# Kernel optimization log

Hardware: AMD Instinct MI355X
Metric: run time of the kernel (lower is better)

The kernel has to match this reference:

```python
import jax, jax.numpy as jnp
import numpy as np

H = 4  # attention heads


def gat_layer(x, src, dst, W, a_src, a_dst, b, N):
    """PyG-style GATConv (concat=True, negative_slope=0.2, eval-mode dropout)."""
    h = (x @ W).reshape(N, H, -1)                       # [N,H,C]
    es = jnp.einsum('nhc,hc->nh', h, a_src)             # per-node src score
    ed = jnp.einsum('nhc,hc->nh', h, a_dst)             # per-node dst score
    e = jax.nn.leaky_relu(es[src] + ed[dst], negative_slope=0.2)  # [E,H]
    # segment softmax over incoming edges of each destination node
    emax = jax.ops.segment_max(e, dst, num_segments=N)
    ee = jnp.exp(e - emax[dst])
    denom = jax.ops.segment_sum(ee, dst, num_segments=N)
    alpha = ee / (denom[dst] + 1e-16)                   # [E,H]
    out = jax.ops.segment_sum(h[src] * alpha[..., None], dst, num_segments=N)
    return out.reshape(N, -1) + b                        # [N,H*C]


def setup_inputs() -> dict:
    key = jax.random.key(0)
    ks = jax.random.split(key, 13)
    N, E, D, Q = 50000, 800000, 256, 8
    HID, OUT = 256, 256
    Ch, Co = HID // H, OUT // H
    inp = {}
    inp['x'] = jax.random.normal(ks[0], (N, D), dtype=jnp.float32)
    inp['edge_index'] = jax.random.randint(ks[1], (2, E), 0, N, dtype=jnp.int64)
    inp['query_embedding'] = jax.random.normal(ks[2], (Q, OUT), dtype=jnp.float32)
    # layer 1: input_dim -> heads * (hidden_dim//heads)
    inp['W1'] = jax.random.normal(ks[3], (D, HID), dtype=jnp.float32) / np.sqrt(D).astype(np.float32)
    inp['a_src1'] = jax.random.normal(ks[4], (H, Ch), dtype=jnp.float32) / np.sqrt(Ch).astype(np.float32)
    inp['a_dst1'] = jax.random.normal(ks[5], (H, Ch), dtype=jnp.float32) / np.sqrt(Ch).astype(np.float32)
    inp['b1'] = jnp.zeros((HID,), dtype=jnp.float32)
    # layer 2: hidden_dim -> heads * (output_dim//heads)
    inp['W2'] = jax.random.normal(ks[6], (HID, OUT), dtype=jnp.float32) / np.sqrt(HID).astype(np.float32)
    inp['a_src2'] = jax.random.normal(ks[7], (H, Co), dtype=jnp.float32) / np.sqrt(Co).astype(np.float32)
    inp['a_dst2'] = jax.random.normal(ks[8], (H, Co), dtype=jnp.float32) / np.sqrt(Co).astype(np.float32)
    inp['b2'] = jnp.zeros((OUT,), dtype=jnp.float32)
    # node classifier over concat([query, node]) -> 1 (intended Linear(2*OUT, 1))
    inp['Wc'] = jax.random.normal(ks[9], (2 * OUT, 1), dtype=jnp.float32) / np.sqrt(2 * OUT).astype(np.float32)
    inp['bc'] = jnp.zeros((1,), dtype=jnp.float32)
    return inp


def reference(x, edge_index, query_embedding, W1, a_src1, a_dst1, b1,
              W2, a_src2, a_dst2, b2, Wc, bc):
    N = x.shape[0]
    loops = jnp.arange(N, dtype=edge_index.dtype)        # GATConv add_self_loops=True
    src = jnp.concatenate([edge_index[0], loops])
    dst = jnp.concatenate([edge_index[1], loops])
    h = jax.nn.relu(gat_layer(x, src, dst, W1, a_src1, a_dst1, b1, N))
    emb = gat_layer(h, src, dst, W2, a_src2, a_dst2, b2, N)  # [N, OUT]
    D = emb.shape[1]
    # scores[q,n] = Linear(concat(query[q], emb[n])) — computed without
    # materializing the [Q,N,2D] concat (identical math).
    q_part = query_embedding @ Wc[:D] + bc               # [Q,1]
    n_part = emb @ Wc[D:]                                # [N,1]
    node_scores = q_part[:, 0][:, None] + n_part[:, 0][None, :]  # [Q,N]
    return emb, node_scores
```

## Files before the change

### kernel.cpp

```cpp
#include <hip/hip_runtime.h>

typedef unsigned short u16;
typedef unsigned int   u32;
typedef __attribute__((ext_vector_type(8))) short short8v;
typedef __attribute__((ext_vector_type(8))) unsigned short us8;
typedef __attribute__((ext_vector_type(4))) float f32x4;

static __device__ __forceinline__ float bf2f(u16 u){ union{u32 i; float f;} v; v.i=(u32)u<<16; return v.f; }
static __device__ __forceinline__ u16 f2bf(float f){ union{float f; u32 i;} u; u.f=f; u32 r=u.i+0x7FFFu+((u.i>>16)&1u); return (u16)(r>>16); }
static __device__ __forceinline__ u32 cvtpk(float lo, float hi){
  u32 r; asm("v_cvt_pk_bf16_f32 %0, %1, %2" : "=v"(r) : "v"(lo), "v"(hi)); return r;
}

static __device__ __forceinline__ float ld1(const void* p, size_t i, int f32){
  return f32 ? ((const float*)p)[i] : bf2f(((const u16*)p)[i]);
}
static __device__ __forceinline__ float4 ld4(const void* p, size_t i, int f32){
  if (f32) return *((const float4*)((const float*)p + i));
  ushort4 v = *((const ushort4*)((const u16*)p + i));
  return make_float4(bf2f(v.x), bf2f(v.y), bf2f(v.z), bf2f(v.w));
}
static __device__ __forceinline__ void st4(void* p, size_t i, float4 v, int f32){
  if (f32) *((float4*)((float*)p + i)) = v;
  else { ushort4 o; o.x=f2bf(v.x); o.y=f2bf(v.y); o.z=f2bf(v.z); o.w=f2bf(v.w); *((ushort4*)((u16*)p + i)) = o; }
}
static __device__ __forceinline__ void st1(void* p, size_t i, float v, int f32){
  if (f32) ((float*)p)[i] = v; else ((u16*)p)[i] = f2bf(v);
}
static __device__ __forceinline__ int lde(const int* ei, size_t i, int i64){
  return i64 ? ei[2*i] : ei[i];
}
static __device__ __forceinline__ int clampi(int v, int lo, int hi){ return v<lo?lo:(v>hi?hi:v); }

__global__ void detect_kernel(const u32* __restrict__ x, const int* __restrict__ ei,
                              int* __restrict__ flags){
  __shared__ int cnt[2];
  int t = threadIdx.x;
  if (t < 2) cnt[t] = 0;
  __syncthreads();
  int good = 0;
  for (int i = t; i < 4096; i += 256){
    u32 e = (x[i] >> 7) & 0xFFu;
    if (e >= 90u && e <= 150u) good++;
  }
  atomicAdd(&cnt[0], good);
  int nzodd = 0;
  for (int i = t; i < 2048; i += 256){
    if (ei[2*i+1] != 0) nzodd++;
  }
  atomicAdd(&cnt[1], nzodd);
  __syncthreads();
  if (t == 0){
    flags[0] = (cnt[0] < 2867) ? 1 : 0;
    flags[1] = (cnt[1] == 0) ? 1 : 0;
  }
}

__global__ __launch_bounds__(256) void convx_kernel(const void* __restrict__ x,
    u16* __restrict__ out, long total, const int* __restrict__ flags){
  if (!flags[0]) return;
  long i = ((long)blockIdx.x*256 + threadIdx.x) * 8;
  if (i >= total) return;
  const float* xf = (const float*)x + i;
  float4 v0 = *(const float4*)xf, v1 = *(const float4*)(xf+4);
  union{ u32 w[4]; us8 v; } pk;
  pk.w[0] = cvtpk(v0.x, v0.y); pk.w[1] = cvtpk(v0.z, v0.w);
  pk.w[2] = cvtpk(v1.x, v1.y); pk.w[3] = cvtpk(v1.z, v1.w);
  *(us8*)(out + i) = pk.v;
}

__global__ void count_kernel(const int* __restrict__ ei, int E, int N,
                             int* __restrict__ deg, const int* __restrict__ flags){
  int i64 = flags[1];
  int i = blockIdx.x*blockDim.x + threadIdx.x;
  int Et = E + N;
  if (i < Et){
    int d = (i < E) ? clampi(lde(ei, (size_t)E + i, i64), 0, N-1) : (i - E);
    atomicAdd(&deg[d], 1);
  }
}

__global__ __launch_bounds__(256) void scan1_kernel(const int* __restrict__ deg,
    int* __restrict__ offs, int* __restrict__ bsum, int N){
  __shared__ int sm[256];
  int t = threadIdx.x;
  int i = blockIdx.x*256 + t;
  int v = (i < N) ? deg[i] : 0;
  sm[t] = v; __syncthreads();
  #pragma unroll
  for (int off = 1; off < 256; off <<= 1){
    int u = (t >= off) ? sm[t-off] : 0;
    __syncthreads();
    sm[t] += u;
    __syncthreads();
  }
  if (i < N) offs[i] = sm[t] - v;
  if (t == 255) bsum[blockIdx.x] = sm[255];
}

__global__ __launch_bounds__(1024) void scan2_kernel(const int* __restrict__ bsum,
    int* __restrict__ bpre, int NB){
  __shared__ int sm[1024];
  int t = threadIdx.x;
  int v = (t < NB) ? bsum[t] : 0;
  sm[t] = v; __syncthreads();
  #pragma unroll
  for (int off = 1; off < 1024; off <<= 1){
    int u = (t >= off) ? sm[t-off] : 0;
    __syncthreads();
    sm[t] += u;
    __syncthreads();
  }
  if (t < NB) bpre[t] = sm[t] - v;
  if (t == 1023) bpre[NB] = sm[1023];
}

__global__ __launch_bounds__(256) void scan3_kernel(int* __restrict__ offs,
    int* __restrict__ cursor, const int* __restrict__ bpre, int N, int NB){
  int i = blockIdx.x*256 + threadIdx.x;
  if (i < N){
    int v = offs[i] + bpre[blockIdx.x];
    offs[i] = v; cursor[i] = v;
  }
  if (i == 0) offs[N] = bpre[NB];
}

__global__ void scatter_kernel(const int* __restrict__ ei, int E, int N,
    int* __restrict__ cursor, int* __restrict__ csr_boff, const int* __restrict__ flags){
  int i64 = flags[1];
  int i = blockIdx.x*blockDim.x + threadIdx.x;
  int Et = E + N;
  if (i < Et){
    int s, d;
    if (i < E){
      s = clampi(lde(ei, i, i64), 0, N-1);
      d = clampi(lde(ei, (size_t)E + i, i64), 0, N-1);
    } else { s = i - E; d = s; }
    int p = atomicAdd(&cursor[d], 1);
    csr_boff[p] = s * 512;
  }
}

__global__ __launch_bounds__(256) void prep_kernel(const void* __restrict__ B1,
    const void* __restrict__ B2, u16* __restrict__ BT1, u16* __restrict__ BT2,
    const void* __restrict__ query, const void* __restrict__ Wc, const void* __restrict__ bc,
    float* __restrict__ qp, int Q, const int* __restrict__ flags){
  int f32 = flags[0];
  int bid = blockIdx.x;
  if (bid < 32){
    const void* B = (bid >= 16) ? B2 : B1;
    u16* BT = (bid >= 16) ? BT2 : BT1;
    int rem = bid & 15;
    int k0 = (rem >> 2)*64, c0 = (rem & 3)*64;
    __shared__ u16 tile[64][65];
    int r0 = threadIdx.x >> 6, c = threadIdx.x & 63;
    for (int r = r0; r < 64; r += 4)
      tile[r][c] = f32 ? f2bf(((const float*)B)[(size_t)(k0+r)*256 + c0 + c])
                       : ((const u16*)B)[(size_t)(k0+r)*256 + c0 + c];
    __syncthreads();
    for (int j = r0; j < 64; j += 4)
      BT[(size_t)(c0+j)*256 + k0 + c] = tile[c][j];
  } else {
    int q = threadIdx.x >> 5, ln = threadIdx.x & 31;
    if (q >= Q) return;
    float s = 0.f;
    for (int j = ln; j < 256; j += 32) s += ld1(query, q*256 + j, f32) * ld1(Wc, j, f32);
    #pragma unroll
    for (int off = 16; off; off >>= 1) s += __shfl_down(s, off, 32);
    if (ln == 0) qp[q] = s + ld1(bc, 0, f32);
  }
}

__global__ __launch_bounds__(256, 4) void gemm_mfma(const u16* __restrict__ A0,
    const u16* __restrict__ A1, const u16* __restrict__ BT, u16* __restrict__ C,
    int M, int aIsInput, const int* __restrict__ flags, float* __restrict__ es,
    float* __restrict__ ed, const void* __restrict__ a_src, const void* __restrict__ a_dst){
  const u16* A16 = (aIsInput && flags[0]) ? A1 : A0;
  int f32 = flags[0];
  int tid = threadIdx.x;
  int wn = tid >> 6, lane = tid & 63;
  int l15 = lane & 15, l4 = lane >> 4;
  int row0 = blockIdx.x * 64;
  int arow[4];
  #pragma unroll
  for (int mi = 0; mi < 4; mi++)
    arow[mi] = min(row0 + mi*16 + l15, M-1);
  const u16* Bb = BT + (size_t)(wn*64 + l15)*256 + 8*l4;
  f32x4 acc[4][4] = {};
  #pragma unroll
  for (int k0 = 0; k0 < 256; k0 += 32){
    short8v a[4], b[4];
    #pragma unroll
    for (int mi = 0; mi < 4; mi++)
      a[mi] = *(const short8v*)(A16 + (size_t)arow[mi]*256 + k0 + 8*l4);
    #pragma unroll
    for (int ni = 0; ni < 4; ni++)
      b[ni] = *(const short8v*)(Bb + (size_t)ni*16*256 + k0);
    #pragma unroll
    for (int mi = 0; mi < 4; mi++)
      #pragma unroll
      for (int ni = 0; ni < 4; ni++)
        acc[mi][ni] = __builtin_amdgcn_mfma_f32_16x16x32_bf16(a[mi], b[ni], acc[mi][ni], 0, 0, 0);
  }
  #pragma unroll
  for (int mi = 0; mi < 4; mi++){
    #pragma unroll
    for (int ni = 0; ni < 4; ni++){
      #pragma unroll
      for (int r = 0; r < 4; r++){
        int row = row0 + mi*16 + l4*4 + r;
        int col = wn*64 + ni*16 + l15;
        if (row < M) C[(size_t)row*256 + col] = f2bf(acc[mi][ni][r]);
      }
    }
  }
  float as_[4], ad_[4];
  #pragma unroll
  for (int ni = 0; ni < 4; ni++){
    as_[ni] = ld1(a_src, wn*64 + ni*16 + l15, f32);
    ad_[ni] = ld1(a_dst, wn*64 + ni*16 + l15, f32);
  }
  #pragma unroll
  for (int mi = 0; mi < 4; mi++){
    #pragma unroll
    for (int r = 0; r < 4; r++){
      float pe = acc[mi][0][r]*as_[0] + acc[mi][1][r]*as_[1]
               + acc[mi][2][r]*as_[2] + acc[mi][3][r]*as_[3];
      float pd = acc[mi][0][r]*ad_[0] + acc[mi][1][r]*ad_[1]
               + acc[mi][2][r]*ad_[2] + acc[mi][3][r]*ad_[3];
      #pragma unroll
      for (int off = 1; off < 16; off <<= 1){
        pe += __shfl_xor(pe, off, 64);
        pd += __shfl_xor(pd, off, 64);
      }
      if (l15 == 0){
        int row = row0 + mi*16 + l4*4 + r;
        if (row < M){
          es[(size_t)row*4 + wn] = pe;
          ed[(size_t)row*4 + wn] = pd;
        }
      }
    }
  }
}

__global__ __launch_bounds__(256) void agg_kernel(const u16* __restrict__ h,
    const int* __restrict__ csr_boff, const int* __restrict__ offs,
    const float* __restrict__ es, const float* __restrict__ ed, int N,
    const void* __restrict__ bias, void* __restrict__ out, int do_relu, int outIsOutput,
    const int* __restrict__ flags, const void* __restrict__ Wc,
    const float* __restrict__ qp, int Q){
  int f32in = flags[0];
  int of32  = outIsOutput ? flags[0] : 0;
  int ln = threadIdx.x & 63;
  int n = blockIdx.x*4 + (threadIdx.x >> 6);
  if (n >= N) return;
  int beg = offs[n], end = offs[n+1];
  int hd = ln >> 4, c0 = ln*4;
  int hd4 = hd*4;
  size_t coff = (size_t)c0*2;
  const char* hbase = (const char*)h;
  const char* ebase = (const char*)es;
  float edn = ed[(size_t)n*4 + hd];
  float a0=0.f, a1=0.f, a2=0.f, a3=0.f, ws=0.f;
  int i = beg;
  for (; i + 8 <= end; i += 8){
    int bo[8]; float x[8]; ushort4 hv[8];
    #pragma unroll
    for (int j = 0; j < 8; j++) bo[j] = csr_boff[i+j];
    #pragma unroll
    for (int j = 0; j < 8; j++) x[j] = *(const float*)(ebase + (bo[j] >> 5) + hd4);
    #pragma unroll
    for (int j = 0; j < 8; j++) hv[j] = *(const ushort4*)(hbase + bo[j] + coff);
    #pragma unroll
    for (int j = 0; j < 8; j++){
      float t = x[j] + edn; t = (t > 0.f) ? t : 0.2f*t; t = fminf(t, 60.f);
      float w = __expf(t);
      a0 += w*bf2f(hv[j].x); a1 += w*bf2f(hv[j].y);
      a2 += w*bf2f(hv[j].z); a3 += w*bf2f(hv[j].w);
      ws += w;
    }
  }
  for (; i + 4 <= end; i += 4){
    int bo[4]; float x[4]; ushort4 hv[4];
    #pragma unroll
    for (int j = 0; j < 4; j++) bo[j] = csr_boff[i+j];
    #pragma unroll
    for (int j = 0; j < 4; j++) x[j] = *(const float*)(ebase + (bo[j] >> 5) + hd4);
    #pragma unroll
    for (int j = 0; j < 4; j++) hv[j] = *(const ushort4*)(hbase + bo[j] + coff);
    #pragma unroll
    for (int j = 0; j < 4; j++){
      float t = x[j] + edn; t = (t > 0.f) ? t : 0.2f*t; t = fminf(t, 60.f);
      float w = __expf(t);
      a0 += w*bf2f(hv[j].x); a1 += w*bf2f(hv[j].y);
      a2 += w*bf2f(hv[j].z); a3 += w*bf2f(hv[j].w);
      ws += w;
    }
  }
  for (; i < end; i++){
    int bo = csr_boff[i];
    float t = *(const float*)(ebase + (bo >> 5) + hd4) + edn;
    t = (t > 0.f) ? t : 0.2f*t; t = fminf(t, 60.f);
    float w = __expf(t);
    ushort4 hv = *(const ushort4*)(hbase + bo + coff);
    a0 += w*bf2f(hv.x); a1 += w*bf2f(hv.y);
    a2 += w*bf2f(hv.z); a3 += w*bf2f(hv.w);
    ws += w;
  }
  float inv = 1.f / (ws + 1e-16f);
  float4 bv = ld4(bias, c0, f32in);
  float4 ov = make_float4(a0*inv + bv.x, a1*inv + bv.y, a2*inv + bv.z, a3*inv + bv.w);
  if (do_relu){
    ov.x = fmaxf(ov.x, 0.f); ov.y = fmaxf(ov.y, 0.f);
    ov.z = fmaxf(ov.z, 0.f); ov.w = fmaxf(ov.w, 0.f);
  }
  st4(out, (size_t)n*256 + c0, ov, of32);
  if (outIsOutput){
    float4 wc4 = ld4(Wc, 256 + c0, f32in);
    float v = ov.x*wc4.x + ov.y*wc4.y + ov.z*wc4.z + ov.w*wc4.w;
    #pragma unroll
    for (int off = 1; off < 64; off <<= 1) v += __shfl_xor(v, off, 64);
    if (ln < Q) st1(out, (size_t)N*256 + (size_t)ln*N + n, qp[ln] + v, of32);
  }
}

extern "C" void kernel_launch(void* const* d_in, const int* in_sizes, int n_in,
                              void* d_out, int out_size, void* d_ws, size_t ws_size,
                              hipStream_t stream){
  const void* x     = d_in[0];
  const int*  ei    = (const int*)d_in[1];
  const void* query = d_in[2];
  const void* W1    = d_in[3];
  const void* as1   = d_in[4];
  const void* ad1   = d_in[5];
  const void* b1    = d_in[6];
  const void* W2    = d_in[7];
  const void* as2   = d_in[8];
  const void* ad2   = d_in[9];
  const void* b2    = d_in[10];
  const void* Wc    = d_in[11];
  const void* bc    = d_in[12];

  int N = in_sizes[0] / 256;
  int E = in_sizes[1] / 2;
  int Q = in_sizes[2] / 256;
  int Et = E + N;
  int NB = (N + 255) / 256;

  char* p = (char*)d_ws;
  auto alloc = [&](size_t bytes)->char*{
    char* r = p; p += (bytes + 255) & ~(size_t)255; return r;
  };
  int*  flags    = (int*) alloc(256);
  u16*  bufA     = (u16*) alloc((size_t)N*256*2);
  u16*  bufB     = (u16*) alloc((size_t)N*256*2);
  u16*  xb       = (u16*) alloc((size_t)N*256*2);
  float* es      = (float*)alloc((size_t)N*4*4);
  float* ed      = (float*)alloc((size_t)N*4*4);
  int*  deg      = (int*)  alloc((size_t)N*4);
  int*  offs     = (int*)  alloc((size_t)(N+1)*4);
  int*  cursor   = (int*)  alloc((size_t)N*4);
  int*  csr_boff = (int*)  alloc((size_t)Et*4);
  int*  bsum     = (int*)  alloc((size_t)(NB+1)*4);
  int*  bpre     = (int*)  alloc((size_t)(NB+1)*4);
  u16*  BT1      = (u16*)  alloc(256*256*2);
  u16*  BT2      = (u16*)  alloc(256*256*2);
  float* qp      = (float*)alloc(64*4);

  const int thr = 256;
  detect_kernel<<<1, 256, 0, stream>>>((const u32*)x, ei, flags);

  hipMemsetAsync(deg, 0, (size_t)N*4, stream);
  count_kernel  <<<(Et + thr-1)/thr, thr, 0, stream>>>(ei, E, N, deg, flags);
  scan1_kernel  <<<NB, 256, 0, stream>>>(deg, offs, bsum, N);
  scan2_kernel  <<<1, 1024, 0, stream>>>(bsum, bpre, NB);
  scan3_kernel  <<<NB, 256, 0, stream>>>(offs, cursor, bpre, N, NB);
  scatter_kernel<<<(Et + thr-1)/thr, thr, 0, stream>>>(ei, E, N, cursor, csr_boff, flags);

  prep_kernel<<<33, 256, 0, stream>>>(W1, W2, BT1, BT2, query, Wc, bc, qp, Q, flags);

  long xtotal = (long)N*256;
  int cxblocks = (int)((xtotal/8 + 255) / 256);
  convx_kernel<<<cxblocks, 256, 0, stream>>>(x, xb, xtotal, flags);

  int gblocks = (N + 63)/64;
  dim3 ngrid((N + 3)/4);

  gemm_mfma <<<gblocks, 256, 0, stream>>>((const u16*)x, xb, BT1, bufA, N, 1, flags,
                                          es, ed, as1, ad1);
  agg_kernel<<<ngrid, 256, 0, stream>>>(bufA, csr_boff, offs, es, ed, N, b1, bufB, 1, 0,
                                        flags, Wc, qp, Q);
  gemm_mfma <<<gblocks, 256, 0, stream>>>(bufB, bufB, BT2, bufA, N, 0, flags,
                                          es, ed, as2, ad2);
  agg_kernel<<<ngrid, 256, 0, stream>>>(bufA, csr_boff, offs, es, ed, N, b2, d_out, 0, 1,
                                        flags, Wc, qp, Q);
}
```

Measured before the change: 348.4 us.

## Stage GEMM tiles in LDS via direct global-to-LDS loads with swizzle

The projection GEMM now uses 512-thread blocks covering 128 rows, with 8 waves arranged 2x4. Per 32-wide K step, the A and B tiles are copied straight into shared memory with global_load_lds and an XOR swizzle to avoid bank conflicts. The MFMA operands then come from LDS rather than separate per-wave global loads. This is meant to cut redundant global/L2 traffic for B, which every wave previously loaded itself, and to improve coalescing. The cost is two barriers per K step with no double buffering, so load latency is not overlapped.

```diff
diff --git a/kernel.cpp b/kernel.cpp
--- a/kernel.cpp
+++ b/kernel.cpp
@@ -10,6 +10,11 @@
 static __device__ __forceinline__ u16 f2bf(float f){ union{float f; u32 i;} u; u.f=f; u32 r=u.i+0x7FFFu+((u.i>>16)&1u); return (u16)(r>>16); }
 static __device__ __forceinline__ u32 cvtpk(float lo, float hi){
   u32 r; asm("v_cvt_pk_bf16_f32 %0, %1, %2" : "=v"(r) : "v"(lo), "v"(hi)); return r;
+}
+static __device__ __forceinline__ void gload16(const u16* g, u16* l){
+  __builtin_amdgcn_global_load_lds(
+      (const __attribute__((address_space(1))) u32*)g,
+      (__attribute__((address_space(3))) u32*)l, 16, 0, 0);
 }
 
 static __device__ __forceinline__ float ld1(const void* p, size_t i, int f32){
@@ -171,31 +176,48 @@
   }
 }
 
-__global__ __launch_bounds__(256, 4) void gemm_mfma(const u16* __restrict__ A0,
+__global__ __launch_bounds__(512, 4) void gemm_mfma(const u16* __restrict__ A0,
     const u16* __restrict__ A1, const u16* __restrict__ BT, u16* __restrict__ C,
     int M, int aIsInput, const int* __restrict__ flags, float* __restrict__ es,
     float* __restrict__ ed, const void* __restrict__ a_src, const void* __restrict__ a_dst){
   const u16* A16 = (aIsInput && flags[0]) ? A1 : A0;
   int f32 = flags[0];
+  __shared__ __align__(16) u16 As[128*32];
+  __shared__ __align__(16) u16 Bs[256*32];
   int tid = threadIdx.x;
-  int wn = tid >> 6, lane = tid & 63;
+  int wave = tid >> 6, lane = tid & 63;
+  int wm = wave >> 2, wn = wave & 3;
   int l15 = lane & 15, l4 = lane >> 4;
-  int row0 = blockIdx.x * 64;
-  int arow[4];
-  #pragma unroll
-  for (int mi = 0; mi < 4; mi++)
-    arow[mi] = min(row0 + mi*16 + l15, M-1);
-  const u16* Bb = BT + (size_t)(wn*64 + l15)*256 + 8*l4;
+  int row0 = blockIdx.x * 128;
+  int arow_s = tid >> 2, apch = tid & 3;
+  int agr = min(row0 + arow_s, M-1);
+  const u16* aSrc = A16 + (size_t)agr*256 + (apch ^ ((arow_s >> 1) & 3))*8;
+  u16* aDst = &As[(size_t)wave*512];
+  int sb0 = (wave*2+0)*64 + lane, sb1 = (wave*2+1)*64 + lane;
+  int bc0 = sb0 >> 2, bp0 = sb0 & 3;
+  int bc1 = sb1 >> 2, bp1 = sb1 & 3;
+  const u16* bSrc0 = BT + (size_t)bc0*256 + (bp0 ^ ((bc0 >> 1) & 3))*8;
+  const u16* bSrc1 = BT + (size_t)bc1*256 + (bp1 ^ ((bc1 >> 1) & 3))*8;
+  u16* bDst0 = &Bs[(size_t)(wave*2+0)*512];
+  u16* bDst1 = &Bs[(size_t)(wave*2+1)*512];
   f32x4 acc[4][4] = {};
-  #pragma unroll
   for (int k0 = 0; k0 < 256; k0 += 32){
+    __syncthreads();
+    gload16(aSrc + k0, aDst);
+    gload16(bSrc0 + k0, bDst0);
+    gload16(bSrc1 + k0, bDst1);
+    __syncthreads();
     short8v a[4], b[4];
     #pragma unroll
-    for (int mi = 0; mi < 4; mi++)
-      a[mi] = *(const short8v*)(A16 + (size_t)arow[mi]*256 + k0 + 8*l4);
-    #pragma unroll
-    for (int ni = 0; ni < 4; ni++)
-      b[ni] = *(const short8v*)(Bb + (size_t)ni*16*256 + k0);
+    for (int mi = 0; mi < 4; mi++){
+      int row = wm*64 + mi*16 + l15;
+      a[mi] = *(const short8v*)&As[row*32 + (l4 ^ ((row >> 1) & 3))*8];
+    }
+    #pragma unroll
+    for (int ni = 0; ni < 4; ni++){
+      int col = wn*64 + ni*16 + l15;
+      b[ni] = *(const short8v*)&Bs[col*32 + (l4 ^ ((col >> 1) & 3))*8];
+    }
     #pragma unroll
     for (int mi = 0; mi < 4; mi++)
       #pragma unroll
@@ -208,7 +230,7 @@
     for (int ni = 0; ni < 4; ni++){
       #pragma unroll
       for (int r = 0; r < 4; r++){
-        int row = row0 + mi*16 + l4*4 + r;
+        int row = row0 + wm*64 + mi*16 + l4*4 + r;
         int col = wn*64 + ni*16 + l15;
         if (row < M) C[(size_t)row*256 + col] = f2bf(acc[mi][ni][r]);
       }
@@ -234,7 +256,7 @@
         pd += __shfl_xor(pd, off, 64);
       }
       if (l15 == 0){
-        int row = row0 + mi*16 + l4*4 + r;
+        int row = row0 + wm*64 + mi*16 + l4*4 + r;
         if (row < M){
           es[(size_t)row*4 + wn] = pe;
           ed[(size_t)row*4 + wn] = pd;
@@ -384,14 +406,14 @@
   int cxblocks = (int)((xtotal/8 + 255) / 256);
   convx_kernel<<<cxblocks, 256, 0, stream>>>(x, xb, xtotal, flags);
 
-  int gblocks = (N + 63)/64;
+  int gblocks = (N + 127)/128;
   dim3 ngrid((N + 3)/4);
 
-  gemm_mfma <<<gblocks, 256, 0, stream>>>((const u16*)x, xb, BT1, bufA, N, 1, flags,
+  gemm_mfma <<<gblocks, 512, 0, stream>>>((const u16*)x, xb, BT1, bufA, N, 1, flags,
                                           es, ed, as1, ad1);
   agg_kernel<<<ngrid, 256, 0, stream>>>(bufA, csr_boff, offs, es, ed, N, b1, bufB, 1, 0,
                                         flags, Wc, qp, Q);
-  gemm_mfma <<<gblocks, 256, 0, stream>>>(bufB, bufB, BT2, bufA, N, 0, flags,
+  gemm_mfma <<<gblocks, 512, 0, stream>>>(bufB, bufB, BT2, bufA, N, 0, flags,
                                           es, ed, as2, ad2);
   agg_kernel<<<ngrid, 256, 0, stream>>>(bufA, csr_boff, offs, es, ed, N, b2, d_out, 0, 1,
                                         flags, Wc, qp, Q);
```

After: 312.7 us. 1.11x faster.
